# Kernel tuning notes

Hardware: AMD Instinct MI355X
Metric: run time of the kernel (lower is better)

Reference implementation:

```python
import jax, jax.numpy as jnp
import numpy as np

D_MODEL = 1024
HEADS = 16
D_K = D_MODEL // HEADS
B, S = 2, 2048


def setup_inputs() -> dict:
    key = jax.random.key(0)
    ks = jax.random.split(key, 11)
    sc = 1.0 / np.sqrt(D_MODEL)
    return {
        "q": jax.random.normal(ks[0], (B, S, D_MODEL), jnp.float32),
        "k": jax.random.normal(ks[1], (B, S, D_MODEL), jnp.float32),
        "v": jax.random.normal(ks[2], (B, S, D_MODEL), jnp.float32),
        "Wq": jax.random.normal(ks[3], (D_MODEL, D_MODEL), jnp.float32) * sc,
        "bq": jnp.zeros((D_MODEL,), jnp.float32),
        "Wk": jax.random.normal(ks[4], (D_MODEL, D_MODEL), jnp.float32) * sc,
        "bk": jnp.zeros((D_MODEL,), jnp.float32),
        "Wv": jax.random.normal(ks[5], (D_MODEL, D_MODEL), jnp.float32) * sc,
        "bv": jnp.zeros((D_MODEL,), jnp.float32),
        "Wo": jax.random.normal(ks[6], (D_MODEL, D_MODEL), jnp.float32) * sc,
        "bo": jnp.zeros((D_MODEL,), jnp.float32),
    }


def reference(q, k, v, Wq, bq, Wk, bk, Wv, bv, Wo, bo):
    bs = q.shape[0]
    # linear projections then split heads: [B,S,D] -> [B,H,S,Dk]
    def proj(x, W, b):
        y = x @ W.T + b
        return y.reshape(bs, -1, HEADS, D_K).transpose(0, 2, 1, 3)

    qh = proj(q, Wq, bq)
    kh = proj(k, Wk, bk)
    vh = proj(v, Wv, bv)
    # scores: [B,H,Sq,Sk] -- full attention matrix as in the original
    scores = jnp.einsum("bhqd,bhkd->bhqk", qh, kh) / jnp.sqrt(
        jnp.asarray(D_K, jnp.float32))
    attn = jax.nn.softmax(scores, axis=-1)
    # dropout is identity in eval/reference mode
    out = jnp.einsum("bhqk,bhkd->bhqd", attn, vh)
    concat = out.transpose(0, 2, 1, 3).reshape(bs, -1, D_MODEL)
    return concat @ Wo.T + bo
```

## Files before the change

kernel.cpp:

```cpp
#include <hip/hip_runtime.h>
#include <hip/hip_bf16.h>

typedef __attribute__((ext_vector_type(8))) short bf16x8;
typedef __attribute__((ext_vector_type(4))) float f32x4;
typedef __attribute__((ext_vector_type(16))) float f32x16;

#define DM   1024
#define SEQ  2048
#define NB   2
#define NH   16
#define MR   (NB*SEQ)

#define SMK  (MR*DM)
#define W1M  (DM*DM)

#define QSCALE 0.18033688011112042f

#define OFF_QB  ((size_t)0)
#define OFF_KB  ((size_t)SMK)
#define OFF_WQB ((size_t)(3*(size_t)SMK))
#define OFF_WO  ((size_t)(3*(size_t)SMK + 3*(size_t)W1M))
#define OFF_QP  ((size_t)(3*(size_t)SMK + 4*(size_t)W1M))
#define OFF_KP  ((size_t)(4*(size_t)SMK + 4*(size_t)W1M))
#define OFF_VP  ((size_t)(5*(size_t)SMK + 4*(size_t)W1M))
#define OFF_CC  ((size_t)0)

__device__ __forceinline__ unsigned short f2bf(float f) {
  union { __hip_bfloat16 b; unsigned short u; } cv;
  cv.b = __float2bfloat16(f);
  return cv.u;
}

__device__ __forceinline__ unsigned int cvtpk_bf16(float lo, float hi) {
  unsigned int r;
  asm("v_cvt_pk_bf16_f32 %0, %1, %2" : "=v"(r) : "v"(lo), "v"(hi));
  return r;
}

__device__ __forceinline__ void plane32_swap(unsigned int& a, unsigned int& b) {
  asm("v_permlane32_swap_b32 %0, %1" : "+v"(a), "+v"(b));
}

__global__ __launch_bounds__(256) void cvt_all(const float* __restrict__ wq,
                                               const float* __restrict__ wk,
                                               const float* __restrict__ wo,
                                               const float* __restrict__ v,
                                               unsigned short* __restrict__ ws) {
  int i = blockIdx.x * 256 + threadIdx.x;
  const float* src;
  unsigned short* dst;
  int j;
  if (i < 3 * (W1M / 4)) {
    int z = i >> 18;
    j = i & ((W1M / 4) - 1);
    src = (z == 0) ? wq : ((z == 1) ? wk : wo);
    dst = ws + ((z == 2) ? OFF_WO : OFF_WQB + (size_t)z * W1M);
  } else {
    j = i - 3 * (W1M / 4);
    src = v;
    dst = ws + OFF_KB;
  }
  float4 val = reinterpret_cast<const float4*>(src)[j];
  ushort4 o;
  o.x = f2bf(val.x); o.y = f2bf(val.y); o.z = f2bf(val.z); o.w = f2bf(val.w);
  reinterpret_cast<ushort4*>(dst)[j] = o;
}

__device__ __forceinline__ void gload_lds16(const void* g, void* l) {
  __builtin_amdgcn_global_load_lds(
      (const __attribute__((address_space(1))) unsigned int*)g,
      (__attribute__((address_space(3))) unsigned int*)l,
      16, 0, 0);
}

template<bool BIAS_ROW>
__device__ __forceinline__ void gemm_hyb_body(unsigned char* __restrict__ Afs,
                                              unsigned short* __restrict__ Bs,
                                              const float* __restrict__ A,
                                              const unsigned short* __restrict__ B,
                                              const float* __restrict__ bias,
                                              unsigned short* __restrict__ C,
                                              int N, int K, float scale,
                                              int brow, int bcol) {
  const int tid  = threadIdx.x;
  const int lane = tid & 63;
  const int w    = tid >> 6;
  const int wr   = w >> 1, wc = w & 1;

  f32x4 acc[4][4];
#pragma unroll
  for (int m = 0; m < 4; m++)
#pragma unroll
    for (int n = 0; n < 4; n++) acc[m][n] = (f32x4){0.f, 0.f, 0.f, 0.f};

  const int arow_l = lane >> 3;
  const int agch   = (lane & 7) ^ arow_l;
  const int srow = lane >> 2;
  const int scol = (lane & 3) * 8;

  auto stage = [&](int buf, int k0) {
#pragma unroll
    for (int ii = 0; ii < 4; ii++) {
      int j = w * 4 + ii;
      gload_lds16(A + (size_t)(brow + j * 8 + arow_l) * K + k0 + agch * 4,
                  Afs + (size_t)buf * 16384 + j * 1024);
    }
#pragma unroll
    for (int c = w; c < 8; c += 4)
      gload_lds16(B + (size_t)(bcol + c * 16 + srow) * K + k0 + scol,
                  (char*)Bs + (size_t)buf * 8192 + c * 1024);
  };

  stage(0, 0);
  stage(1, 32);

  const int nk = K / 32;
  const int g      = lane >> 4;
  const int lrow_a = wr * 64 + (lane & 15);
  const int lrow_b = wc * 64 + (lane & 15);
  const int lcol   = g * 8;
  const int s0 = (2 * g) ^ (lane & 7);
  const int s1 = (2 * g + 1) ^ (lane & 7);

  int b0 = 0;
  for (int kt = 0; kt < nk; ++kt) {
    if (kt + 1 < nk) asm volatile("s_waitcnt vmcnt(6)" ::: "memory");
    else             asm volatile("s_waitcnt vmcnt(0)" ::: "memory");
    __builtin_amdgcn_s_barrier();
    __builtin_amdgcn_sched_barrier(0);
    if (kt + 2 < nk) {
      int bn = b0 + 2; if (bn >= 3) bn -= 3;
      stage(bn, (kt + 2) * 32);
    }
    const unsigned char* Ab = Afs + (size_t)b0 * 16384;
    bf16x8 a[4], b[4];
#pragma unroll
    for (int m = 0; m < 4; m++) {
      int R = lrow_a + m * 16;
      f32x4 lo = *(const f32x4*)(Ab + R * 128 + s0 * 16);
      f32x4 hi = *(const f32x4*)(Ab + R * 128 + s1 * 16);
      union { unsigned int u[4]; bf16x8 v8; } ua;
      ua.u[0] = cvtpk_bf16(lo[0], lo[1]);
      ua.u[1] = cvtpk_bf16(lo[2], lo[3]);
      ua.u[2] = cvtpk_bf16(hi[0], hi[1]);
      ua.u[3] = cvtpk_bf16(hi[2], hi[3]);
      a[m] = ua.v8;
    }
#pragma unroll
    for (int n = 0; n < 4; n++)
      b[n] = *(const bf16x8*)&Bs[(size_t)b0 * 4096 + (lrow_b + n * 16) * 32 + lcol];
    __builtin_amdgcn_s_setprio(1);
#pragma unroll
    for (int m = 0; m < 4; m++)
#pragma unroll
      for (int n = 0; n < 4; n++)
        acc[m][n] = __builtin_amdgcn_mfma_f32_16x16x32_bf16(a[m], b[n], acc[m][n], 0, 0, 0);
    __builtin_amdgcn_s_setprio(0);
    b0 = (b0 == 2) ? 0 : b0 + 1;
  }

  const int crow0 = brow + wr * 64;
  const int ccol0 = bcol + wc * 64;
  const int rsub  = (lane >> 4) * 4;
  const int csub  = lane & 15;
#pragma unroll
  for (int m = 0; m < 4; m++)
#pragma unroll
    for (int n = 0; n < 4; n++) {
      int col = ccol0 + n * 16 + csub;
      float bcol_v = BIAS_ROW ? 0.f : bias[col];
#pragma unroll
      for (int qq = 0; qq < 4; qq++) {
        int row = crow0 + m * 16 + rsub + qq;
        float bb = BIAS_ROW ? bias[row] : bcol_v;
        C[(size_t)row * N + col] = f2bf((acc[m][n][qq] + bb) * scale);
      }
    }
}

__global__ __launch_bounds__(256, 2) void gemm_qkv(const float* __restrict__ q,
                                                   const float* __restrict__ k,
                                                   const float* __restrict__ Wv,
                                                   unsigned short* ws,
                                                   const float* __restrict__ bq,
                                                   const float* __restrict__ bk,
                                                   const float* __restrict__ bv) {
  __shared__ __align__(16) unsigned char Afs[3 * 16384];
  __shared__ unsigned short Bs[3 * 4096];
  const int i  = blockIdx.x;
  const int x  = i & 7;
  const int r  = i >> 3;
  const int pm = r >> 3;
  const int bx = r & 7;
  const int p  = x * 12 + pm;
  const int z  = p >> 5;
  const int by = p & 31;
  if (z < 2) {
    gemm_hyb_body<false>(Afs, Bs,
                         z ? k : q, ws + OFF_WQB + (size_t)z * W1M, z ? bk : bq,
                         ws + OFF_QP + (size_t)z * SMK,
                         DM, DM, z ? 1.f : QSCALE, by * 128, bx * 128);
  } else {
    gemm_hyb_body<true>(Afs, Bs,
                        Wv, ws + OFF_KB, bv,
                        ws + OFF_VP,
                        MR, DM, 1.f, bx * 128, by * 128);
  }
}

__device__ __forceinline__ void gemm_out_body(unsigned short* __restrict__ As,
                                              unsigned short* __restrict__ Bs,
                                              const unsigned short* __restrict__ A,
                                              const unsigned short* __restrict__ Bt,
                                              const float* __restrict__ bias,
                                              float* __restrict__ Cv,
                                              int N, int K,
                                              int brow, int bcol) {
  constexpr int BM = 64, BN = 128;
  const int tid  = threadIdx.x;
  const int lane = tid & 63;
  const int w    = tid >> 6;
  const int wr   = w >> 1, wc = w & 1;

  f32x4 acc[2][4];
#pragma unroll
  for (int m = 0; m < 2; m++)
#pragma unroll
    for (int n = 0; n < 4; n++) acc[m][n] = (f32x4){0.f, 0.f, 0.f, 0.f};

  const int srow = lane >> 2;
  const int scol = (lane & 3) * 8;

  auto stage = [&](int buf, int k0) {
#pragma unroll
    for (int c = w; c < BM / 16; c += 4)
      gload_lds16(A + (size_t)(brow + c * 16 + srow) * K + k0 + scol,
                  (char*)As + (size_t)buf * BM * 64 + c * 1024);
#pragma unroll
    for (int c = w; c < BN / 16; c += 4)
      gload_lds16(Bt + (size_t)(bcol + c * 16 + srow) * K + k0 + scol,
                  (char*)Bs + (size_t)buf * BN * 64 + c * 1024);
  };

  stage(0, 0);
  stage(1, 32);

  const int nk = K / 32;
  const int lrow_a = wr * (BM / 2) + (lane & 15);
  const int lrow_b = wc * (BN / 2) + (lane & 15);
  const int lcol   = (lane >> 4) * 8;

  int b0 = 0;
  for (int kt = 0; kt < nk; ++kt) {
    if (kt + 1 < nk) asm volatile("s_waitcnt vmcnt(3)" ::: "memory");
    else             asm volatile("s_waitcnt vmcnt(0)" ::: "memory");
    __builtin_amdgcn_s_barrier();
    __builtin_amdgcn_sched_barrier(0);
    if (kt + 2 < nk) {
      int bn = b0 + 2; if (bn >= 3) bn -= 3;
      stage(bn, (kt + 2) * 32);
    }
    bf16x8 a[2], b[4];
#pragma unroll
    for (int m = 0; m < 2; m++)
      a[m] = *(const bf16x8*)&As[(size_t)b0 * BM * 32 + (lrow_a + m * 16) * 32 + lcol];
#pragma unroll
    for (int n = 0; n < 4; n++)
      b[n] = *(const bf16x8*)&Bs[(size_t)b0 * BN * 32 + (lrow_b + n * 16) * 32 + lcol];
    __builtin_amdgcn_s_setprio(1);
#pragma unroll
    for (int m = 0; m < 2; m++)
#pragma unroll
      for (int n = 0; n < 4; n++)
        acc[m][n] = __builtin_amdgcn_mfma_f32_16x16x32_bf16(a[m], b[n], acc[m][n], 0, 0, 0);
    __builtin_amdgcn_s_setprio(0);
    b0 = (b0 == 2) ? 0 : b0 + 1;
  }

  const int crow0 = brow + wr * (BM / 2);
  const int ccol0 = bcol + wc * (BN / 2);
  const int rsub  = (lane >> 4) * 4;
  const int csub  = lane & 15;
#pragma unroll
  for (int m = 0; m < 2; m++)
#pragma unroll
    for (int n = 0; n < 4; n++) {
      int col = ccol0 + n * 16 + csub;
      float bv = bias[col];
#pragma unroll
      for (int qq = 0; qq < 4; qq++) {
        int row = crow0 + m * 16 + rsub + qq;
        Cv[(size_t)row * N + col] = acc[m][n][qq] + bv;
      }
    }
}

__global__ __launch_bounds__(256) void gemm_out(const unsigned short* __restrict__ ws,
                                                const float* __restrict__ bo,
                                                float* __restrict__ out) {
  __shared__ unsigned short As[3 * 64 * 32];
  __shared__ unsigned short Bs[3 * 128 * 32];
  const int i  = blockIdx.x;
  const int x  = i & 7;
  const int r  = i >> 3;
  const int pm = r >> 3;
  const int bx = r & 7;
  const int by = x * 8 + pm;
  gemm_out_body(As, Bs,
                ws + OFF_CC, ws + OFF_WO, bo, out,
                DM, DM, by * 64, bx * 128);
}

__global__ __launch_bounds__(512, 4) void flash_attn(unsigned short* ws) {
  __shared__ __align__(16) unsigned char smem[65536];

  const int tid  = threadIdx.x;
  const int lane = tid & 63;
  const int w    = tid >> 6;
  const int s    = w >> 2;
  const int wsub = w & 3;
  const int q    = lane & 31;
  const int hi   = lane >> 5;
  const int swq  = q & 7;
  const int bid  = blockIdx.x;
  const int swzb = (bid & 7) * 64 + (bid >> 3);
  const int qblk = swzb & 15;
  const int bh   = swzb >> 4;
  const int b    = bh >> 4, h = bh & 15;

  const unsigned short* Qp = ws + OFF_QP;
  const unsigned short* Kp = ws + OFF_KP;
  const unsigned short* Vp = ws + OFF_VP;
  unsigned short* CC = ws + OFF_CC;

  const unsigned short* Kg = Kp + (size_t)(b * SEQ) * DM + h * 64;
  const unsigned short* Vg = Vp + (size_t)(h * 64) * MR + (size_t)b * SEQ;

  bf16x8 bqf[4];
  {
    const unsigned short* qrow =
        Qp + (size_t)(b * SEQ + qblk * 128 + wsub * 32 + q) * DM + h * 64;
#pragma unroll
    for (int c = 0; c < 4; c++)
      bqf[c] = *(const bf16x8*)(qrow + c * 16 + hi * 8);
  }

  f32x16 o_acc[2];
#pragma unroll
  for (int dt = 0; dt < 2; dt++)
#pragma unroll
    for (int r = 0; r < 16; r++) o_acc[dt][r] = 0.f;
  float l_run = 0.f;

  auto stage = [&](int buf, int t) {
    const unsigned short* Kt = Kg + (size_t)(s * 16 + t) * 64 * DM;
    const unsigned short* Vt = Vg + (s * 16 + t) * 64;
    char* base = (char*)smem + (size_t)(s * 2 + buf) * 16384;
#pragma unroll
    for (int i = 0; i < 2; i++) {
      int slot = wsub * 128 + i * 64 + lane;
      int srow = slot >> 3;
      int gch  = (slot & 7) ^ (srow & 7);
      gload_lds16(Kt + (size_t)srow * DM + gch * 8, base + slot * 16);
      gload_lds16(Vt + (size_t)srow * MR + gch * 8, base + 8192 + slot * 16);
    }
  };

  stage(0, 0);

  for (int t = 0; t < 16; ++t) {
    int buf = t & 1;
    __syncthreads();
    if (t + 1 < 16) stage(buf ^ 1, t + 1);
    const unsigned short* Kb = (const unsigned short*)(smem + (size_t)(s * 2 + buf) * 16384);
    const unsigned short* Vb = Kb + 4096;

    f32x16 st0, st1;
#pragma unroll
    for (int r = 0; r < 16; r++) { st0[r] = 0.f; st1[r] = 0.f; }
    __builtin_amdgcn_s_setprio(1);
#pragma unroll
    for (int c = 0; c < 4; c++) {
      int ch = (((c << 1) | hi) ^ swq) << 3;
      bf16x8 ak0 = *(const bf16x8*)&Kb[q * 64 + ch];
      bf16x8 ak1 = *(const bf16x8*)&Kb[(32 + q) * 64 + ch];
      st0 = __builtin_amdgcn_mfma_f32_32x32x16_bf16(ak0, bqf[c], st0, 0, 0, 0);
      st1 = __builtin_amdgcn_mfma_f32_32x32x16_bf16(ak1, bqf[c], st1, 0, 0, 0);
    }
    __builtin_amdgcn_s_setprio(0);

    unsigned int pk0[8], pk1[8];
    float lt = 0.f;
#pragma unroll
    for (int p = 0; p < 8; p++) {
      float a0 = __builtin_amdgcn_exp2f(st0[2 * p]);
      float a1 = __builtin_amdgcn_exp2f(st0[2 * p + 1]);
      float b0 = __builtin_amdgcn_exp2f(st1[2 * p]);
      float b1 = __builtin_amdgcn_exp2f(st1[2 * p + 1]);
      lt += (a0 + a1) + (b0 + b1);
      pk0[p] = cvtpk_bf16(a0, a1);
      pk1[p] = cvtpk_bf16(b0, b1);
    }
    l_run += lt;

    plane32_swap(pk0[0], pk0[2]); plane32_swap(pk0[1], pk0[3]);
    plane32_swap(pk0[4], pk0[6]); plane32_swap(pk0[5], pk0[7]);
    plane32_swap(pk1[0], pk1[2]); plane32_swap(pk1[1], pk1[3]);
    plane32_swap(pk1[4], pk1[6]); plane32_swap(pk1[5], pk1[7]);

    __builtin_amdgcn_s_setprio(1);
#pragma unroll
    for (int t4 = 0; t4 < 4; t4++) {
      union { unsigned int u[4]; bf16x8 v; } pb;
      const unsigned int* src = (t4 < 2) ? pk0 : pk1;
      pb.u[0] = src[(t4 & 1) * 4 + 0];
      pb.u[1] = src[(t4 & 1) * 4 + 1];
      pb.u[2] = src[(t4 & 1) * 4 + 2];
      pb.u[3] = src[(t4 & 1) * 4 + 3];
      int ch = (((t4 << 1) | hi) ^ swq) << 3;
#pragma unroll
      for (int dt = 0; dt < 2; dt++) {
        bf16x8 av = *(const bf16x8*)&Vb[(dt * 32 + q) * 64 + ch];
        o_acc[dt] = __builtin_amdgcn_mfma_f32_32x32x16_bf16(av, pb.v, o_acc[dt], 0, 0, 0);
      }
    }
    __builtin_amdgcn_s_setprio(0);
  }

  __syncthreads();
  float* scr = (float*)smem;
  float lsum = l_run + __shfl_xor(l_run, 32, 64);
  if (s == 1) {
    int idx = (wsub * 64 + lane) * 33;
#pragma unroll
    for (int dt = 0; dt < 2; dt++)
#pragma unroll
      for (int r = 0; r < 16; r++) scr[idx + dt * 16 + r] = o_acc[dt][r];
    scr[idx + 32] = lsum;
  }
  __syncthreads();
  if (s == 0) {
    int idx = (wsub * 64 + lane) * 33;
#pragma unroll
    for (int dt = 0; dt < 2; dt++)
#pragma unroll
      for (int r = 0; r < 16; r++) o_acc[dt][r] += scr[idx + dt * 16 + r];
    float l = lsum + scr[idx + 32];
    float inv = 1.f / l;

    int qg = b * SEQ + qblk * 128 + wsub * 32 + q;
    unsigned short* crow = CC + (size_t)qg * DM + h * 64;
#pragma unroll
    for (int dt = 0; dt < 2; dt++)
#pragma unroll
      for (int rq = 0; rq < 4; rq++) {
        ushort4 o;
        o.x = f2bf(o_acc[dt][4 * rq + 0] * inv);
        o.y = f2bf(o_acc[dt][4 * rq + 1] * inv);
        o.z = f2bf(o_acc[dt][4 * rq + 2] * inv);
        o.w = f2bf(o_acc[dt][4 * rq + 3] * inv);
        *(ushort4*)&crow[dt * 32 + rq * 8 + hi * 4] = o;
      }
  }
}

extern "C" void kernel_launch(void* const* d_in, const int* in_sizes, int n_in,
                              void* d_out, int out_size, void* d_ws, size_t ws_size,
                              hipStream_t stream) {
  const float* q  = (const float*)d_in[0];
  const float* k  = (const float*)d_in[1];
  const float* v  = (const float*)d_in[2];
  const float* Wq = (const float*)d_in[3];
  const float* bq = (const float*)d_in[4];
  const float* Wk = (const float*)d_in[5];
  const float* bk = (const float*)d_in[6];
  const float* Wv = (const float*)d_in[7];
  const float* bv = (const float*)d_in[8];
  const float* Wo = (const float*)d_in[9];
  const float* bo = (const float*)d_in[10];

  unsigned short* ws = (unsigned short*)d_ws;
  float* out = (float*)d_out;

  cvt_all<<<dim3((3 * (W1M / 4) + SMK / 4) / 256), dim3(256), 0, stream>>>(
      Wq, Wk, Wo, v, ws);

  gemm_qkv<<<dim3(768), dim3(256), 0, stream>>>(q, k, Wv, ws, bq, bk, bv);

  flash_attn<<<dim3(512), dim3(512), 0, stream>>>(ws);

  gemm_out<<<dim3(512), dim3(256), 0, stream>>>(ws, bo, out);
}
```

Measured before the change: 130.1 us.

## Convert fp32 A tiles to bf16 in registers before LDS in QKV GEMM

The QKV projection GEMM used to copy fp32 A tiles straight into a triple-buffered LDS via direct global-to-LDS loads and convert them to bf16 on every fragment read. It now loads A into registers two tiles ahead, converts to bf16 once, and writes half-size bf16 tiles into a double-buffered LDS, while B keeps the direct LDS loads. This cuts LDS footprint and read traffic so the launch bound can rise from 2 to 3 blocks per CU. The cost is more register pressure and VGPR staging of A, plus tighter double-buffer synchronisation.

```diff
diff --git a/kernel.cpp b/kernel.cpp
--- a/kernel.cpp
+++ b/kernel.cpp
@@ -74,14 +74,14 @@
 }
 
 template<bool BIAS_ROW>
-__device__ __forceinline__ void gemm_hyb_body(unsigned char* __restrict__ Afs,
-                                              unsigned short* __restrict__ Bs,
-                                              const float* __restrict__ A,
-                                              const unsigned short* __restrict__ B,
-                                              const float* __restrict__ bias,
-                                              unsigned short* __restrict__ C,
-                                              int N, int K, float scale,
-                                              int brow, int bcol) {
+__device__ __forceinline__ void gemm_hyb2_body(unsigned short* __restrict__ As,
+                                               unsigned short* __restrict__ Bs,
+                                               const float* __restrict__ A,
+                                               const unsigned short* __restrict__ B,
+                                               const float* __restrict__ bias,
+                                               unsigned short* __restrict__ C,
+                                               int N, int K, float scale,
+                                               int brow, int bcol) {
   const int tid  = threadIdx.x;
   const int lane = tid & 63;
   const int w    = tid >> 6;
@@ -93,62 +93,68 @@
 #pragma unroll
     for (int n = 0; n < 4; n++) acc[m][n] = (f32x4){0.f, 0.f, 0.f, 0.f};
 
-  const int arow_l = lane >> 3;
-  const int agch   = (lane & 7) ^ arow_l;
   const int srow = lane >> 2;
   const int scol = (lane & 3) * 8;
 
-  auto stage = [&](int buf, int k0) {
-#pragma unroll
-    for (int ii = 0; ii < 4; ii++) {
-      int j = w * 4 + ii;
-      gload_lds16(A + (size_t)(brow + j * 8 + arow_l) * K + k0 + agch * 4,
-                  Afs + (size_t)buf * 16384 + j * 1024);
-    }
+  f32x4 ra0[2][2], ra1[2][2];
+
+  auto loadA = [&](int k0, f32x4 (&fa)[2][2]) {
+#pragma unroll
+    for (int i = 0; i < 2; i++) {
+      const float* pa = A + (size_t)(brow + (w + i * 4) * 16 + srow) * K + k0 + scol;
+      fa[i][0] = *(const f32x4*)pa;
+      fa[i][1] = *(const f32x4*)(pa + 4);
+    }
+  };
+  auto commitA = [&](int buf, f32x4 (&fa)[2][2]) {
+#pragma unroll
+    for (int i = 0; i < 2; i++) {
+      union { unsigned int u[4]; bf16x8 v8; } ua;
+#pragma unroll
+      for (int j = 0; j < 2; j++) {
+        ua.u[2 * j]     = cvtpk_bf16(fa[i][j][0], fa[i][j][1]);
+        ua.u[2 * j + 1] = cvtpk_bf16(fa[i][j][2], fa[i][j][3]);
+      }
+      *(bf16x8*)((char*)As + (size_t)buf * 8192 + (w + i * 4) * 1024 + lane * 16) = ua.v8;
+    }
+  };
+  auto stageB = [&](int buf, int k0) {
 #pragma unroll
     for (int c = w; c < 8; c += 4)
       gload_lds16(B + (size_t)(bcol + c * 16 + srow) * K + k0 + scol,
                   (char*)Bs + (size_t)buf * 8192 + c * 1024);
   };
 
-  stage(0, 0);
-  stage(1, 32);
-
   const int nk = K / 32;
-  const int g      = lane >> 4;
+
+  loadA(0, ra0);
+  commitA(0, ra0);
+  loadA(32, ra1);
+  stageB(0, 0);
+  loadA(64, ra0);
+
   const int lrow_a = wr * 64 + (lane & 15);
   const int lrow_b = wc * 64 + (lane & 15);
-  const int lcol   = g * 8;
-  const int s0 = (2 * g) ^ (lane & 7);
-  const int s1 = (2 * g + 1) ^ (lane & 7);
-
-  int b0 = 0;
-  for (int kt = 0; kt < nk; ++kt) {
-    if (kt + 1 < nk) asm volatile("s_waitcnt vmcnt(6)" ::: "memory");
-    else             asm volatile("s_waitcnt vmcnt(0)" ::: "memory");
+  const int lcol   = (lane >> 4) * 8;
+
+  auto iter = [&](int kt, f32x4 (&rs)[2][2]) {
+    if (kt + 2 < nk) asm volatile("s_waitcnt vmcnt(4) lgkmcnt(0)" ::: "memory");
+    else             asm volatile("s_waitcnt vmcnt(0) lgkmcnt(0)" ::: "memory");
     __builtin_amdgcn_s_barrier();
     __builtin_amdgcn_sched_barrier(0);
-    if (kt + 2 < nk) {
-      int bn = b0 + 2; if (bn >= 3) bn -= 3;
-      stage(bn, (kt + 2) * 32);
-    }
-    const unsigned char* Ab = Afs + (size_t)b0 * 16384;
+    int buf = kt & 1;
     bf16x8 a[4], b[4];
 #pragma unroll
-    for (int m = 0; m < 4; m++) {
-      int R = lrow_a + m * 16;
-      f32x4 lo = *(const f32x4*)(Ab + R * 128 + s0 * 16);
-      f32x4 hi = *(const f32x4*)(Ab + R * 128 + s1 * 16);
-      union { unsigned int u[4]; bf16x8 v8; } ua;
-      ua.u[0] = cvtpk_bf16(lo[0], lo[1]);
-      ua.u[1] = cvtpk_bf16(lo[2], lo[3]);
-      ua.u[2] = cvtpk_bf16(hi[0], hi[1]);
-      ua.u[3] = cvtpk_bf16(hi[2], hi[3]);
-      a[m] = ua.v8;
-    }
+    for (int m = 0; m < 4; m++)
+      a[m] = *(const bf16x8*)&As[(size_t)buf * 4096 + (lrow_a + m * 16) * 32 + lcol];
 #pragma unroll
     for (int n = 0; n < 4; n++)
-      b[n] = *(const bf16x8*)&Bs[(size_t)b0 * 4096 + (lrow_b + n * 16) * 32 + lcol];
+      b[n] = *(const bf16x8*)&Bs[(size_t)buf * 4096 + (lrow_b + n * 16) * 32 + lcol];
+    if (kt + 1 < nk) {
+      commitA(buf ^ 1, rs);
+      stageB(buf ^ 1, (kt + 1) * 32);
+    }
+    if (kt + 3 < nk) loadA((kt + 3) * 32, rs);
     __builtin_amdgcn_s_setprio(1);
 #pragma unroll
     for (int m = 0; m < 4; m++)
@@ -156,7 +162,11 @@
       for (int n = 0; n < 4; n++)
         acc[m][n] = __builtin_amdgcn_mfma_f32_16x16x32_bf16(a[m], b[n], acc[m][n], 0, 0, 0);
     __builtin_amdgcn_s_setprio(0);
-    b0 = (b0 == 2) ? 0 : b0 + 1;
+  };
+
+  for (int kt = 0; kt < nk; kt += 2) {
+    iter(kt,     ra1);
+    iter(kt + 1, ra0);
   }
 
   const int crow0 = brow + wr * 64;
@@ -178,15 +188,15 @@
     }
 }
 
-__global__ __launch_bounds__(256, 2) void gemm_qkv(const float* __restrict__ q,
+__global__ __launch_bounds__(256, 3) void gemm_qkv(const float* __restrict__ q,
                                                    const float* __restrict__ k,
                                                    const float* __restrict__ Wv,
                                                    unsigned short* ws,
                                                    const float* __restrict__ bq,
                                                    const float* __restrict__ bk,
                                                    const float* __restrict__ bv) {
-  __shared__ __align__(16) unsigned char Afs[3 * 16384];
-  __shared__ unsigned short Bs[3 * 4096];
+  __shared__ unsigned short As[2 * 128 * 32];
+  __shared__ unsigned short Bs[2 * 128 * 32];
   const int i  = blockIdx.x;
   const int x  = i & 7;
   const int r  = i >> 3;
@@ -196,15 +206,15 @@
   const int z  = p >> 5;
   const int by = p & 31;
   if (z < 2) {
-    gemm_hyb_body<false>(Afs, Bs,
-                         z ? k : q, ws + OFF_WQB + (size_t)z * W1M, z ? bk : bq,
-                         ws + OFF_QP + (size_t)z * SMK,
-                         DM, DM, z ? 1.f : QSCALE, by * 128, bx * 128);
+    gemm_hyb2_body<false>(As, Bs,
+                          z ? k : q, ws + OFF_WQB + (size_t)z * W1M, z ? bk : bq,
+                          ws + OFF_QP + (size_t)z * SMK,
+                          DM, DM, z ? 1.f : QSCALE, by * 128, bx * 128);
   } else {
-    gemm_hyb_body<true>(Afs, Bs,
-                        Wv, ws + OFF_KB, bv,
-                        ws + OFF_VP,
-                        MR, DM, 1.f, bx * 128, by * 128);
+    gemm_hyb2_body<true>(As, Bs,
+                         Wv, ws + OFF_KB, bv,
+                         ws + OFF_VP,
+                         MR, DM, 1.f, bx * 128, by * 128);
   }
 }
 
```

Result: faster. 110.6 us, median of 3 (-15.0%).

## Replace LDS-staged QKV GEMM with register-direct 32x32 MFMA loads

Applied to the files above, without the earlier changes.

The QKV projection GEMM no longer stages A and B tiles through shared memory with a triple-buffered async pipeline. Each wave now loads its fp32 A rows and bf16 B rows straight from global memory into registers, software-pipelined two steps ahead, and uses 32x32x16 MFMAs. Without LDS the occupancy hint rises to 4 blocks per CU. The cost is that tiles are no longer shared between waves through LDS, so each B tile is read separately by all four waves and each load is a narrower strided row access, which adds global and L2 traffic.

```diff
diff --git a/kernel.cpp b/kernel.cpp
--- a/kernel.cpp
+++ b/kernel.cpp
@@ -74,119 +74,86 @@
 }
 
 template<bool BIAS_ROW>
-__device__ __forceinline__ void gemm_hyb_body(unsigned char* __restrict__ Afs,
-                                              unsigned short* __restrict__ Bs,
-                                              const float* __restrict__ A,
-                                              const unsigned short* __restrict__ B,
-                                              const float* __restrict__ bias,
-                                              unsigned short* __restrict__ C,
-                                              int N, int K, float scale,
-                                              int brow, int bcol) {
-  const int tid  = threadIdx.x;
-  const int lane = tid & 63;
-  const int w    = tid >> 6;
-  const int wr   = w >> 1, wc = w & 1;
-
-  f32x4 acc[4][4];
-#pragma unroll
-  for (int m = 0; m < 4; m++)
-#pragma unroll
-    for (int n = 0; n < 4; n++) acc[m][n] = (f32x4){0.f, 0.f, 0.f, 0.f};
-
-  const int arow_l = lane >> 3;
-  const int agch   = (lane & 7) ^ arow_l;
-  const int srow = lane >> 2;
-  const int scol = (lane & 3) * 8;
-
-  auto stage = [&](int buf, int k0) {
-#pragma unroll
-    for (int ii = 0; ii < 4; ii++) {
-      int j = w * 4 + ii;
-      gload_lds16(A + (size_t)(brow + j * 8 + arow_l) * K + k0 + agch * 4,
-                  Afs + (size_t)buf * 16384 + j * 1024);
-    }
-#pragma unroll
-    for (int c = w; c < 8; c += 4)
-      gload_lds16(B + (size_t)(bcol + c * 16 + srow) * K + k0 + scol,
-                  (char*)Bs + (size_t)buf * 8192 + c * 1024);
+__device__ __forceinline__ void gemm_nolds_body(const float* __restrict__ A,
+                                                const unsigned short* __restrict__ B,
+                                                const float* __restrict__ bias,
+                                                unsigned short* __restrict__ C,
+                                                int N, int K, float scale,
+                                                int arow0, int bcol0) {
+  const int lane = threadIdx.x & 63;
+  const int w    = threadIdx.x >> 6;
+  const int q    = lane & 31;
+  const int hi   = lane >> 5;
+
+  f32x16 acc[4];
+#pragma unroll
+  for (int n = 0; n < 4; n++)
+#pragma unroll
+    for (int r = 0; r < 16; r++) acc[n][r] = 0.f;
+
+  const float* pa = A + (size_t)(arow0 + w * 32 + q) * K + hi * 8;
+  const unsigned short* pb = B + (size_t)(bcol0 + q) * K + hi * 8;
+
+  f32x4 a0[2], a1[2];
+  bf16x8 bfr[4];
+
+  auto loadA = [&](int kt, f32x4 (&a)[2]) {
+    const float* p = pa + kt * 16;
+    a[0] = *(const f32x4*)p;
+    a[1] = *(const f32x4*)(p + 4);
   };
-
-  stage(0, 0);
-  stage(1, 32);
-
-  const int nk = K / 32;
-  const int g      = lane >> 4;
-  const int lrow_a = wr * 64 + (lane & 15);
-  const int lrow_b = wc * 64 + (lane & 15);
-  const int lcol   = g * 8;
-  const int s0 = (2 * g) ^ (lane & 7);
-  const int s1 = (2 * g + 1) ^ (lane & 7);
-
-  int b0 = 0;
-  for (int kt = 0; kt < nk; ++kt) {
-    if (kt + 1 < nk) asm volatile("s_waitcnt vmcnt(6)" ::: "memory");
-    else             asm volatile("s_waitcnt vmcnt(0)" ::: "memory");
-    __builtin_amdgcn_s_barrier();
-    __builtin_amdgcn_sched_barrier(0);
-    if (kt + 2 < nk) {
-      int bn = b0 + 2; if (bn >= 3) bn -= 3;
-      stage(bn, (kt + 2) * 32);
-    }
-    const unsigned char* Ab = Afs + (size_t)b0 * 16384;
-    bf16x8 a[4], b[4];
-#pragma unroll
-    for (int m = 0; m < 4; m++) {
-      int R = lrow_a + m * 16;
-      f32x4 lo = *(const f32x4*)(Ab + R * 128 + s0 * 16);
-      f32x4 hi = *(const f32x4*)(Ab + R * 128 + s1 * 16);
-      union { unsigned int u[4]; bf16x8 v8; } ua;
-      ua.u[0] = cvtpk_bf16(lo[0], lo[1]);
-      ua.u[1] = cvtpk_bf16(lo[2], lo[3]);
-      ua.u[2] = cvtpk_bf16(hi[0], hi[1]);
-      ua.u[3] = cvtpk_bf16(hi[2], hi[3]);
-      a[m] = ua.v8;
-    }
+  auto loadB = [&](int kt) {
+    const unsigned short* p = pb + kt * 16;
 #pragma unroll
     for (int n = 0; n < 4; n++)
-      b[n] = *(const bf16x8*)&Bs[(size_t)b0 * 4096 + (lrow_b + n * 16) * 32 + lcol];
+      bfr[n] = *(const bf16x8*)(p + (size_t)n * 32 * K);
+  };
+
+  const int nk = K / 16;
+  loadA(0, a0);
+  loadB(0);
+  loadA(1, a1);
+
+  auto iter = [&](int kt, f32x4 (&ac)[2], f32x4 (&an)[2]) {
+    union { unsigned int u[4]; bf16x8 v8; } ua;
+    ua.u[0] = cvtpk_bf16(ac[0][0], ac[0][1]);
+    ua.u[1] = cvtpk_bf16(ac[0][2], ac[0][3]);
+    ua.u[2] = cvtpk_bf16(ac[1][0], ac[1][1]);
+    ua.u[3] = cvtpk_bf16(ac[1][2], ac[1][3]);
     __builtin_amdgcn_s_setprio(1);
 #pragma unroll
-    for (int m = 0; m < 4; m++)
-#pragma unroll
-      for (int n = 0; n < 4; n++)
-        acc[m][n] = __builtin_amdgcn_mfma_f32_16x16x32_bf16(a[m], b[n], acc[m][n], 0, 0, 0);
+    for (int n = 0; n < 4; n++)
+      acc[n] = __builtin_amdgcn_mfma_f32_32x32x16_bf16(ua.v8, bfr[n], acc[n], 0, 0, 0);
     __builtin_amdgcn_s_setprio(0);
-    b0 = (b0 == 2) ? 0 : b0 + 1;
-  }
-
-  const int crow0 = brow + wr * 64;
-  const int ccol0 = bcol + wc * 64;
-  const int rsub  = (lane >> 4) * 4;
-  const int csub  = lane & 15;
-#pragma unroll
-  for (int m = 0; m < 4; m++)
-#pragma unroll
-    for (int n = 0; n < 4; n++) {
-      int col = ccol0 + n * 16 + csub;
-      float bcol_v = BIAS_ROW ? 0.f : bias[col];
-#pragma unroll
-      for (int qq = 0; qq < 4; qq++) {
-        int row = crow0 + m * 16 + rsub + qq;
-        float bb = BIAS_ROW ? bias[row] : bcol_v;
-        C[(size_t)row * N + col] = f2bf((acc[m][n][qq] + bb) * scale);
-      }
-    }
-}
-
-__global__ __launch_bounds__(256, 2) void gemm_qkv(const float* __restrict__ q,
+    if (kt + 1 < nk) loadB(kt + 1);
+    if (kt + 2 < nk) loadA(kt + 2, ac);
+  };
+
+  for (int kt = 0; kt < nk; kt += 2) {
+    iter(kt,     a0, a1);
+    iter(kt + 1, a1, a0);
+  }
+
+#pragma unroll
+  for (int n = 0; n < 4; n++) {
+    int col = bcol0 + n * 32 + q;
+    float bcv = BIAS_ROW ? 0.f : bias[col];
+#pragma unroll
+    for (int r = 0; r < 16; r++) {
+      int row = arow0 + w * 32 + (r & 3) + 8 * (r >> 2) + 4 * hi;
+      float bb = BIAS_ROW ? bias[row] : bcv;
+      C[(size_t)row * N + col] = f2bf((acc[n][r] + bb) * scale);
+    }
+  }
+}
+
+__global__ __launch_bounds__(256, 4) void gemm_qkv(const float* __restrict__ q,
                                                    const float* __restrict__ k,
                                                    const float* __restrict__ Wv,
                                                    unsigned short* ws,
                                                    const float* __restrict__ bq,
                                                    const float* __restrict__ bk,
                                                    const float* __restrict__ bv) {
-  __shared__ __align__(16) unsigned char Afs[3 * 16384];
-  __shared__ unsigned short Bs[3 * 4096];
   const int i  = blockIdx.x;
   const int x  = i & 7;
   const int r  = i >> 3;
@@ -196,15 +163,13 @@
   const int z  = p >> 5;
   const int by = p & 31;
   if (z < 2) {
-    gemm_hyb_body<false>(Afs, Bs,
-                         z ? k : q, ws + OFF_WQB + (size_t)z * W1M, z ? bk : bq,
-                         ws + OFF_QP + (size_t)z * SMK,
-                         DM, DM, z ? 1.f : QSCALE, by * 128, bx * 128);
+    gemm_nolds_body<false>(z ? k : q, ws + OFF_WQB + (size_t)z * W1M, z ? bk : bq,
+                           ws + OFF_QP + (size_t)z * SMK,
+                           DM, DM, z ? 1.f : QSCALE, by * 128, bx * 128);
   } else {
-    gemm_hyb_body<true>(Afs, Bs,
-                        Wv, ws + OFF_KB, bv,
-                        ws + OFF_VP,
-                        MR, DM, 1.f, bx * 128, by * 128);
+    gemm_nolds_body<true>(Wv, ws + OFF_KB, bv,
+                          ws + OFF_VP,
+                          MR, DM, 1.f, bx * 128, by * 128);
   }
 }
 
```

New measurement: 202.6 us. +55.7%, slower.
